# Performance work log

Measured on AMD Instinct MI355X. Metric: run time of the kernel, lower is better.

The kernel has to match this reference:

```python
import jax, jax.numpy as jnp
import numpy as np

B, T = 8, 8192
D_X, D_H, D_K, D_V = 256, 512, 128, 128
RES_DIMS = [128, 128, 128, 128]
R = sum(RES_DIMS)
MEM_SLOTS, EP_TOPK = 256, 8
LN_EPS = 1e-5


def _ln(x, g, b):
    m = x.mean(-1, keepdims=True)
    v = ((x - m) ** 2).mean(-1, keepdims=True)
    return (x - m) * jax.lax.rsqrt(v + LN_EPS) * g + b


def _l2norm(x, eps=1e-8):
    return x / jnp.maximum(jnp.linalg.norm(x, axis=-1, keepdims=True), eps)


def setup_inputs() -> dict:
    key = jax.random.key(0)
    ks = jax.random.split(key, 12)
    def w(k, shape):  # xavier-ish scaling
        return jax.random.normal(k, shape, jnp.float32) * (shape[-1] ** -0.5)
    return dict(
        x_seq=jax.random.normal(ks[0], (B, T, D_X), jnp.float32),
        Wx_w=w(ks[1], (R, D_X)), Wx_b=jnp.zeros((R,), jnp.float32),
        Wh_w=w(ks[2], (R, D_H)),
        res_alpha=jnp.full((len(RES_DIMS),), -1.0, jnp.float32),
        A_scale=jnp.ones((D_H,), jnp.float32),
        B_w=w(ks[3], (D_H, R)),
        U_w=w(ks[4], (D_H, D_X)), U_b=jnp.zeros((D_H,), jnp.float32),
        fftn_g=jnp.ones((D_H,), jnp.float32), fftn_b=jnp.zeros((D_H,), jnp.float32),
        fftp_w=w(ks[5], (D_H, D_H)), fftp_b=jnp.zeros((D_H,), jnp.float32),
        fft_mix=jnp.asarray(0.5, jnp.float32),
        mix_logit=jnp.asarray(0.0, jnp.float32),
        key_w=w(ks[6], (D_K, R + D_X)), key_b=jnp.zeros((D_K,), jnp.float32),
        val_w=w(ks[7], (D_V, D_H)), val_b=jnp.zeros((D_V,), jnp.float32),
        rm_w=w(ks[8], (D_H, D_V)), rm_b=jnp.zeros((D_H,), jnp.float32),
        rn_g=jnp.ones((R,), jnp.float32), rn_b=jnp.zeros((R,), jnp.float32),
        mem_keys=jax.random.normal(ks[9], (B, MEM_SLOTS, D_K), jnp.float32),
        mem_vals=jax.random.normal(ks[10], (B, MEM_SLOTS, D_K), jnp.float32),
        heb_H=jax.random.normal(ks[11], (B, D_K, D_V), jnp.float32) * 0.1,
    )


def reference(x_seq, Wx_w, Wx_b, Wh_w, res_alpha, A_scale, B_w, U_w, U_b,
              fftn_g, fftn_b, fftp_w, fftp_b, fft_mix, mix_logit,
              key_w, key_b, val_w, val_b, rm_w, rm_b, rn_g, rn_b,
              mem_keys, mem_vals, heb_H):
    b = x_seq.shape[0]
    seg_index = np.repeat(np.arange(len(RES_DIMS)), RES_DIMS)  # static (R,)
    h_prev = jnp.zeros((b, D_H), x_seq.dtype)  # h0 = None
    r_prev = jnp.zeros((b, R), x_seq.dtype)    # r0 = None

    # reservoir update (fully parallel over T since h_prev/r_prev are broadcast)
    Wx = jnp.einsum('btx,rx->btr', x_seq, Wx_w) + Wx_b
    Wh = (h_prev @ Wh_w.T)[:, None, :]                    # (B,1,R), no bias in fwd
    alpha = jax.nn.sigmoid(res_alpha)[seg_index]          # (R,)
    r_seq = alpha * r_prev[:, None, :] + (1.0 - alpha) * jnp.tanh(Wx + Wh)
    r_seq = _ln(r_seq, rn_g, rn_b)

    # core state
    Ah = A_scale * h_prev[:, None, :]
    Bh = jnp.einsum('btr,hr->bth', r_seq, B_w)
    Uh = jnp.einsum('btx,hx->bth', x_seq, U_w) + U_b
    h_tilde = jax.nn.gelu(Ah + Bh + Uh, approximate=False)

    # FFT feature mixing
    h_norm = _ln(h_tilde, fftn_g, fftn_b)
    s = jax.nn.sigmoid(fft_mix)
    h_freq = jnp.fft.rfft(h_norm, n=D_H, axis=-1, norm='ortho')
    h_ifft = jnp.fft.irfft(h_freq * s, n=D_H, axis=-1, norm='ortho')
    h_fft_out = jnp.einsum('bth,oh->bto', h_ifft, fftp_w) + fftp_b
    hs = (1.0 - s) * h_tilde + s * h_fft_out

    # memory recall (once per sequence, batched)
    k = jnp.einsum('btf,kf->btk', jnp.concatenate([r_seq, x_seq], axis=-1), key_w) + key_b
    v = jnp.einsum('bth,vh->btv', hs, val_w) + val_b  # as in original (used for auto_write)
    c = _l2norm(k)
    q = c.mean(axis=1)                                # (B,d_k)

    # episodic: cosine top-k over slots, softmax-weighted value read
    kn = _l2norm(mem_keys)
    sim = jnp.einsum('bk,bmk->bm', _l2norm(q), kn)
    top_sim, top_idx = jax.lax.top_k(sim, EP_TOPK)
    w_att = jax.nn.softmax(top_sim, axis=-1)
    vals = jnp.take_along_axis(mem_vals, top_idx[..., None], axis=1)  # (B,topk,d_v)
    v_hat = jnp.einsum('bk,bkv->bv', w_att, vals)

    # hebbian: linear associative read from per-batch outer-product memory
    v_hebb = jnp.einsum('bk,bkv->bv', q, heb_H)

    mix = jax.nn.sigmoid(mix_logit)
    v_comb = mix * v_hat + (1.0 - mix) * v_hebb
    h_mem = v_comb @ rm_w.T + rm_b                    # (B,d_h)
    hs = hs + 0.5 * h_mem[:, None, :]
    return hs, r_seq
```

## Files before the change

### kernel.cpp

```cpp
#include <hip/hip_runtime.h>
#include <cmath>


typedef __attribute__((ext_vector_type(8)))  short short8;
typedef __attribute__((ext_vector_type(16))) float f32x16;

__device__ __forceinline__ unsigned short f2bf(float f) {
  union { float f; unsigned u; } v; v.f = f;
  unsigned r = v.u + 0x7FFF + ((v.u >> 16) & 1);
  return (unsigned short)(r >> 16);
}
__device__ __forceinline__ float bf2f(unsigned short h) {
  union { unsigned u; float f; } v; v.u = ((unsigned)h) << 16; return v.f;
}
__device__ __forceinline__ f32x16 mfma16(short8 a, short8 b, f32x16 c) {
  return __builtin_amdgcn_mfma_f32_32x32x16_bf16(a, b, c, 0, 0, 0);
}
__device__ __forceinline__ void barrier_lgkm() {
  asm volatile("s_waitcnt lgkmcnt(0)" ::: "memory");
  __builtin_amdgcn_s_barrier();
  __builtin_amdgcn_sched_barrier(0);
}

__global__ __launch_bounds__(256) void k_wconv(
    const float* __restrict__ wx, const float* __restrict__ key,
    const float* __restrict__ bw, const float* __restrict__ uw,
    const float* __restrict__ fftpw, const float* __restrict__ fg,
    unsigned short* __restrict__ wxp, unsigned short* __restrict__ keyp,
    unsigned short* __restrict__ bwp, unsigned short* __restrict__ uwp,
    unsigned short* __restrict__ fftps) {
  int i = blockIdx.x * 256 + threadIdx.x;
  if (i >= 884736) return;
  float v; int n, k, N; unsigned short* dst;
  if (i < 131072)      { int j = i;          N = 512; k = j & 255; n = j >> 8; v = wx[j];  dst = wxp; }
  else if (i < 229376) { int j = i - 131072; N = 128; k = j % 768; n = j / 768; v = key[j]; dst = keyp; }
  else if (i < 491520) { int j = i - 229376; N = 512; k = j & 511; n = j >> 9; v = bw[j];  dst = bwp; }
  else if (i < 622592) { int j = i - 491520; N = 512; k = j & 255; n = j >> 8; v = uw[j];  dst = uwp; }
  else                 { int j = i - 622592; N = 512; k = j & 511; n = j >> 9; v = fftpw[j] * fg[k]; dst = fftps; }
  dst[(k >> 5) * (N * 32) + ((k >> 3) & 3) * (N * 8) + n * 8 + (k & 7)] = f2bf(v);
}

__global__ __launch_bounds__(512, 4) void k_rk(
    const float* __restrict__ x, const unsigned short* __restrict__ wxp,
    const unsigned short* __restrict__ keyp,
    const float* __restrict__ wxb, const float* __restrict__ resa,
    const float* __restrict__ rng, const float* __restrict__ rnb,
    const float* __restrict__ keyb,
    float* __restrict__ rout, float* __restrict__ partial) {
  __shared__ short sX[8192];
  __shared__ short sR[16384];
  __shared__ float red[640];
  const int t = threadIdx.x, w = t >> 6, lane = t & 63, lr = lane & 31, lh = lane >> 5;
  const int m0 = blockIdx.x * 32;

#pragma unroll
  for (int i = 0; i < 4; ++i) {
    int c = t + i * 512;
    int row = c >> 6, k0 = (c & 63) * 4;
    float4 v = *reinterpret_cast<const float4*>(x + (size_t)(m0 + row) * 256 + k0);
    uint2 p;
    p.x = (unsigned)f2bf(v.x) | ((unsigned)f2bf(v.y) << 16);
    p.y = (unsigned)f2bf(v.z) | ((unsigned)f2bf(v.w) << 16);
    *reinterpret_cast<uint2*>(&sX[(k0 >> 3) * 256 + row * 8 + (k0 & 7)]) = p;
  }
  barrier_lgkm();

  f32x16 acc[2];
#pragma unroll
  for (int ni = 0; ni < 2; ++ni)
#pragma unroll
    for (int e = 0; e < 16; ++e) acc[ni][e] = 0.f;
  short8 b0[4], b1[4];
  auto loadB0 = [&](int s, short8 (&bd)[4]) {
#pragma unroll
    for (int kh = 0; kh < 2; ++kh)
#pragma unroll
      for (int ni = 0; ni < 2; ++ni)
        bd[kh * 2 + ni] = *reinterpret_cast<const short8*>(
            wxp + (size_t)s * 16384 + (kh * 2 + lh) * 4096 + (64 * w + 32 * ni + lr) * 8);
  };
  auto mf0 = [&](int s, short8 (&bc)[4]) {
    short8 af[2];
#pragma unroll
    for (int kh = 0; kh < 2; ++kh)
      af[kh] = *reinterpret_cast<const short8*>(&sX[(s * 4 + kh * 2 + lh) * 256 + lr * 8]);
    __builtin_amdgcn_s_setprio(1);
#pragma unroll
    for (int kh = 0; kh < 2; ++kh)
#pragma unroll
      for (int ni = 0; ni < 2; ++ni)
        acc[ni] = mfma16(af[kh], bc[kh * 2 + ni], acc[ni]);
    __builtin_amdgcn_s_setprio(0);
  };
  loadB0(0, b0);
  for (int s = 0; s < 8; s += 2) {
    loadB0(s + 1, b1);
    mf0(s, b0);
    if (s + 2 < 8) loadB0(s + 2, b0);
    mf0(s + 1, b1);
  }

#pragma unroll
  for (int ni = 0; ni < 2; ++ni) {
    int col = 64 * w + 32 * ni + lr;
    float al = 1.f / (1.f + expf(-resa[col >> 7]));
    float oma = 1.f - al, bbv = wxb[col];
#pragma unroll
    for (int r = 0; r < 16; ++r)
      acc[ni][r] = oma * tanhf(acc[ni][r] + bbv);
  }
#pragma unroll
  for (int r = 0; r < 16; ++r) {
    float s1 = acc[0][r] + acc[1][r];
    float s2 = acc[0][r] * acc[0][r] + acc[1][r] * acc[1][r];
#pragma unroll
    for (int m = 1; m <= 16; m <<= 1) { s1 += __shfl_xor(s1, m); s2 += __shfl_xor(s2, m); }
    int rl = (r & 3) + 8 * (r >> 2) + 4 * lh;
    if (lr == r) { red[w * 32 + rl] = s1; red[256 + w * 32 + rl] = s2; }
  }
  __syncthreads();
  if (t < 32) {
    float s1 = 0.f, s2 = 0.f;
#pragma unroll
    for (int n = 0; n < 8; ++n) { s1 += red[n * 32 + t]; s2 += red[256 + n * 32 + t]; }
    float mean = s1 * (1.f / 512.f);
    float var = s2 * (1.f / 512.f) - mean * mean;
    float rstd = rsqrtf(var + 1e-5f);
    red[512 + t * 2] = mean;
    red[512 + t * 2 + 1] = rstd;
  }
  __syncthreads();
#pragma unroll
  for (int q = 0; q < 4; ++q) {
    float4 stA = *reinterpret_cast<float4*>(&red[512 + (8 * q + 4 * lh) * 2]);
    float4 stB = *reinterpret_cast<float4*>(&red[512 + (8 * q + 4 * lh) * 2 + 4]);
    float mean[4] = {stA.x, stA.z, stB.x, stB.z};
    float rstd[4] = {stA.y, stA.w, stB.y, stB.w};
#pragma unroll
    for (int ni = 0; ni < 2; ++ni) {
      int col = 64 * w + 32 * ni + lr;
      float g = rng[col], bbv = rnb[col];
#pragma unroll
      for (int e = 0; e < 4; ++e) {
        int r = 4 * q + e;
        int rloc = 8 * q + 4 * lh + e;
        float val = (acc[ni][r] - mean[e]) * rstd[e] * g + bbv;
        rout[(size_t)(m0 + rloc) * 512 + col] = val;
        sR[(col >> 3) * 256 + rloc * 8 + (col & 7)] = (short)f2bf(val);
      }
    }
  }
  barrier_lgkm();

  const int g = w >> 2, nw2 = w & 3;
  f32x16 ak;
#pragma unroll
  for (int e = 0; e < 16; ++e) ak[e] = 0.f;
  short8 kb0[2], kb1[2];
  auto loadBk = [&](int gc, short8 (&bd)[2]) {
#pragma unroll
    for (int kh = 0; kh < 2; ++kh)
      bd[kh] = *reinterpret_cast<const short8*>(
          keyp + (size_t)gc * 4096 + (kh * 2 + lh) * 1024 + (32 * nw2 + lr) * 8);
  };
  auto mfk = [&](int gc, short8 (&bc)[2]) {
    const short* P = (gc < 16) ? sR : sX;
    int sb = (gc < 16) ? gc * 4 : (gc - 16) * 4;
    short8 af[2];
#pragma unroll
    for (int kh = 0; kh < 2; ++kh)
      af[kh] = *reinterpret_cast<const short8*>(&P[(sb + kh * 2 + lh) * 256 + lr * 8]);
    __builtin_amdgcn_s_setprio(1);
#pragma unroll
    for (int kh = 0; kh < 2; ++kh)
      ak = mfma16(af[kh], bc[kh], ak);
    __builtin_amdgcn_s_setprio(0);
  };
  const int gbase = g * 12;
  loadBk(gbase, kb0);
  for (int s = 0; s < 12; s += 2) {
    loadBk(gbase + s + 1, kb1);
    mfk(gbase + s, kb0);
    if (s + 2 < 12) loadBk(gbase + s + 2, kb0);
    mfk(gbase + s + 1, kb1);
  }
  __syncthreads();
  float* kp = reinterpret_cast<float*>(sR);
#pragma unroll
  for (int r = 0; r < 16; ++r) {
    int rr = (r & 3) + 8 * (r >> 2) + 4 * lh;
    kp[g * 4096 + rr * 128 + nw2 * 32 + lr] = ak[r];
  }
  __syncthreads();
  {
    int rr = t >> 4, cg = t & 15;
    float s1 = 0.f;
#pragma unroll
    for (int j = 0; j < 8; ++j) {
      int c = cg * 8 + j;
      float v = kp[rr * 128 + c] + kp[4096 + rr * 128 + c] + keyb[c];
      s1 += v * v;
    }
#pragma unroll
    for (int m = 1; m <= 8; m <<= 1) s1 += __shfl_xor(s1, m);
    if (cg == 0) red[rr] = 1.f / fmaxf(sqrtf(s1), 1e-8f);
  }
  __syncthreads();
  if (t < 128) {
    float p = 0.f;
    float bb = keyb[t];
#pragma unroll 4
    for (int rr = 0; rr < 32; ++rr)
      p += (kp[rr * 128 + t] + kp[4096 + rr * 128 + t] + bb) * red[rr];
    partial[(size_t)blockIdx.x * 128 + t] = p;
  }
}

__global__ __launch_bounds__(256) void k_qred(const float* __restrict__ partial,
                                              float* __restrict__ q_ws) {
  int gid = blockIdx.x * 256 + threadIdx.x;
  int b = gid >> 7, c = gid & 127;
  float s = 0.f;
  for (int i = 0; i < 256; ++i) s += partial[(size_t)(b * 256 + i) * 128 + c];
  q_ws[gid] = s * (1.f / 8192.f);
}

__global__ __launch_bounds__(256) void k_cvec(const float* __restrict__ fb,
                                              const float* __restrict__ fftpw,
                                              float* __restrict__ cvec) {
  int o = blockIdx.x * 256 + threadIdx.x;
  const float* w = fftpw + (size_t)o * 512;
  float s = 0.f;
  for (int k = 0; k < 512; ++k) s += fb[k] * w[k];
  cvec[o] = s;
}

__global__ __launch_bounds__(256) void k_mem(
    const float* __restrict__ q_ws, const float* __restrict__ mkeys,
    const float* __restrict__ mvals, const float* __restrict__ hebH,
    const float* __restrict__ rmw, const float* __restrict__ rmb,
    const float* __restrict__ mixl, float* __restrict__ hm) {
  const int b = blockIdx.x, t = threadIdx.x;
  __shared__ float qv[128];
  __shared__ float ssim[256];
  __shared__ float red[256];
  __shared__ float tval[8];
  __shared__ int tidx[8];
  __shared__ float wsm[8];
  __shared__ float vcs[128];

  if (t < 128) qv[t] = q_ws[b * 128 + t];
  __syncthreads();
  red[t] = (t < 128) ? qv[t] * qv[t] : 0.f;
  __syncthreads();
  for (int s = 128; s > 0; s >>= 1) {
    if (t < s) red[t] += red[t + s];
    __syncthreads();
  }
  float qsc = 1.f / fmaxf(sqrtf(red[0]), 1e-8f);
  {
    const float* mk = mkeys + ((size_t)b * 256 + t) * 128;
    float dot = 0.f, ms = 0.f;
    for (int k = 0; k < 128; ++k) { float mv = mk[k]; dot += qv[k] * mv; ms += mv * mv; }
    ssim[t] = dot * qsc / fmaxf(sqrtf(ms), 1e-8f);
  }
  __syncthreads();
  for (int it = 0; it < 8; ++it) {
    if (t < 64) {
      float bv = -1e30f; int bi = 0;
#pragma unroll
      for (int u = 0; u < 4; ++u) {
        int m = t * 4 + u;
        float v = ssim[m];
        if (v > bv) { bv = v; bi = m; }
      }
      for (int off = 32; off; off >>= 1) {
        float ov = __shfl_xor(bv, off, 64);
        int oi = __shfl_xor(bi, off, 64);
        if (ov > bv || (ov == bv && oi < bi)) { bv = ov; bi = oi; }
      }
      if (t == 0) { tval[it] = bv; tidx[it] = bi; ssim[bi] = -1e30f; }
    }
    __syncthreads();
  }
  if (t == 0) {
    float m0 = tval[0], sum = 0.f, e[8];
#pragma unroll
    for (int i = 0; i < 8; ++i) { e[i] = expf(tval[i] - m0); sum += e[i]; }
#pragma unroll
    for (int i = 0; i < 8; ++i) wsm[i] = e[i] / sum;
  }
  __syncthreads();
  float mix = 1.f / (1.f + expf(-mixl[0]));
  if (t < 128) {
    float vh = 0.f;
#pragma unroll
    for (int i = 0; i < 8; ++i) vh += wsm[i] * mvals[((size_t)b * 256 + tidx[i]) * 128 + t];
    float vhb = 0.f;
    const float* H = hebH + (size_t)b * 128 * 128;
    for (int k = 0; k < 128; ++k) vhb += qv[k] * H[k * 128 + t];
    vcs[t] = mix * vh + (1.f - mix) * vhb;
  }
  __syncthreads();
  for (int h = t; h < 512; h += 256) {
    float sum = rmb[h];
    const float* wr = rmw + (size_t)h * 128;
    for (int v = 0; v < 128; ++v) sum += vcs[v] * wr[v];
    hm[b * 512 + h] = sum;
  }
}

__global__ __launch_bounds__(512, 4) void k_fused(
    const float* __restrict__ rseq, const float* __restrict__ x,
    const unsigned short* __restrict__ bwp, const unsigned short* __restrict__ uwp,
    const float* __restrict__ ub, const unsigned short* __restrict__ fftps,
    const float* __restrict__ fftpb, const float* __restrict__ fmix,
    const float* __restrict__ cvec, const float* __restrict__ hm,
    float* __restrict__ hs) {
  __shared__ short sX[8192];
  __shared__ short sR[16384];
  __shared__ float red[640];
  const int t = threadIdx.x, w = t >> 6, lane = t & 63, lr = lane & 31, lh = lane >> 5;
  const int m0 = blockIdx.x * 32;
  const int bidx = m0 >> 13;

#pragma unroll
  for (int i = 0; i < 8; ++i) {
    int c = t + i * 512;
    int row = c >> 7, k0 = (c & 127) * 4;
    float4 v = *reinterpret_cast<const float4*>(rseq + (size_t)(m0 + row) * 512 + k0);
    uint2 p;
    p.x = (unsigned)f2bf(v.x) | ((unsigned)f2bf(v.y) << 16);
    p.y = (unsigned)f2bf(v.z) | ((unsigned)f2bf(v.w) << 16);
    *reinterpret_cast<uint2*>(&sR[(k0 >> 3) * 256 + row * 8 + (k0 & 7)]) = p;
  }
#pragma unroll
  for (int i = 0; i < 4; ++i) {
    int c = t + i * 512;
    int row = c >> 6, k0 = (c & 63) * 4;
    float4 v = *reinterpret_cast<const float4*>(x + (size_t)(m0 + row) * 256 + k0);
    uint2 p;
    p.x = (unsigned)f2bf(v.x) | ((unsigned)f2bf(v.y) << 16);
    p.y = (unsigned)f2bf(v.z) | ((unsigned)f2bf(v.w) << 16);
    *reinterpret_cast<uint2*>(&sX[(k0 >> 3) * 256 + row * 8 + (k0 & 7)]) = p;
  }
  barrier_lgkm();

  f32x16 acc[2];
#pragma unroll
  for (int ni = 0; ni < 2; ++ni)
#pragma unroll
    for (int e = 0; e < 16; ++e) acc[ni][e] = 0.f;
  short8 b0[4], b1[4];
  auto loadB1 = [&](int s, short8 (&bd)[4]) {
    const unsigned short* wp = (s < 16) ? (bwp + (size_t)s * 16384)
                                        : (uwp + (size_t)(s - 16) * 16384);
#pragma unroll
    for (int kh = 0; kh < 2; ++kh)
#pragma unroll
      for (int ni = 0; ni < 2; ++ni)
        bd[kh * 2 + ni] = *reinterpret_cast<const short8*>(
            wp + (kh * 2 + lh) * 4096 + (64 * w + 32 * ni + lr) * 8);
  };
  auto mf1 = [&](int s, short8 (&bc)[4]) {
    const short* P = (s < 16) ? sR : sX;
    int sb = (s < 16) ? s * 4 : (s - 16) * 4;
    short8 af[2];
#pragma unroll
    for (int kh = 0; kh < 2; ++kh)
      af[kh] = *reinterpret_cast<const short8*>(&P[(sb + kh * 2 + lh) * 256 + lr * 8]);
    __builtin_amdgcn_s_setprio(1);
#pragma unroll
    for (int kh = 0; kh < 2; ++kh)
#pragma unroll
      for (int ni = 0; ni < 2; ++ni)
        acc[ni] = mfma16(af[kh], bc[kh * 2 + ni], acc[ni]);
    __builtin_amdgcn_s_setprio(0);
  };
  loadB1(0, b0);
  for (int s = 0; s < 24; s += 2) {
    loadB1(s + 1, b1);
    mf1(s, b0);
    if (s + 2 < 24) loadB1(s + 2, b0);
    mf1(s + 1, b1);
  }

#pragma unroll
  for (int ni = 0; ni < 2; ++ni) {
    int col = 64 * w + 32 * ni + lr;
    float ubc = ub[col];
#pragma unroll
    for (int r = 0; r < 16; ++r) {
      float pre = acc[ni][r] + ubc;
      acc[ni][r] = 0.5f * pre * (1.f + erff(pre * 0.70710678118654752f));
    }
  }
#pragma unroll
  for (int r = 0; r < 16; ++r) {
    float s1 = acc[0][r] + acc[1][r];
    float s2 = acc[0][r] * acc[0][r] + acc[1][r] * acc[1][r];
#pragma unroll
    for (int m = 1; m <= 16; m <<= 1) { s1 += __shfl_xor(s1, m); s2 += __shfl_xor(s2, m); }
    int rl = (r & 3) + 8 * (r >> 2) + 4 * lh;
    if (lr == r) { red[w * 32 + rl] = s1; red[256 + w * 32 + rl] = s2; }
  }
  __syncthreads();
  if (t < 32) {
    float s1 = 0.f, s2 = 0.f;
#pragma unroll
    for (int n = 0; n < 8; ++n) { s1 += red[n * 32 + t]; s2 += red[256 + n * 32 + t]; }
    float mean = s1 * (1.f / 512.f);
    float var = s2 * (1.f / 512.f) - mean * mean;
    float rstd = rsqrtf(var + 1e-5f);
    red[512 + t * 2] = mean;
    red[512 + t * 2 + 1] = rstd;
  }
  __syncthreads();
  unsigned htp[2][8];
#pragma unroll
  for (int ni = 0; ni < 2; ++ni)
#pragma unroll
    for (int p = 0; p < 8; ++p)
      htp[ni][p] = (unsigned)f2bf(acc[ni][2 * p]) |
                   ((unsigned)f2bf(acc[ni][2 * p + 1]) << 16);
  auto loadB2 = [&](int s, short8 (&bd)[4]) {
#pragma unroll
    for (int kh = 0; kh < 2; ++kh)
#pragma unroll
      for (int ni = 0; ni < 2; ++ni)
        bd[kh * 2 + ni] = *reinterpret_cast<const short8*>(
            fftps + (size_t)s * 16384 + (kh * 2 + lh) * 4096 + (64 * w + 32 * ni + lr) * 8);
  };
  loadB2(0, b0);
#pragma unroll
  for (int q = 0; q < 4; ++q) {
    float4 stA = *reinterpret_cast<float4*>(&red[512 + (8 * q + 4 * lh) * 2]);
    float4 stB = *reinterpret_cast<float4*>(&red[512 + (8 * q + 4 * lh) * 2 + 4]);
    float mean[4] = {stA.x, stA.z, stB.x, stB.z};
    float rstd[4] = {stA.y, stA.w, stB.y, stB.w};
#pragma unroll
    for (int ni = 0; ni < 2; ++ni) {
      int col = 64 * w + 32 * ni + lr;
#pragma unroll
      for (int e = 0; e < 4; ++e) {
        int r = 4 * q + e;
        float z = (acc[ni][r] - mean[e]) * rstd[e];
        int rloc = 8 * q + 4 * lh + e;
        sR[(col >> 3) * 256 + rloc * 8 + (col & 7)] = (short)f2bf(z);
      }
    }
  }
#pragma unroll
  for (int ni = 0; ni < 2; ++ni)
#pragma unroll
    for (int e = 0; e < 16; ++e) acc[ni][e] = 0.f;
  barrier_lgkm();

  auto mf2 = [&](int s, short8 (&bc)[4]) {
    short8 af[2];
#pragma unroll
    for (int kh = 0; kh < 2; ++kh)
      af[kh] = *reinterpret_cast<const short8*>(&sR[(s * 4 + kh * 2 + lh) * 256 + lr * 8]);
    __builtin_amdgcn_s_setprio(1);
#pragma unroll
    for (int kh = 0; kh < 2; ++kh)
#pragma unroll
      for (int ni = 0; ni < 2; ++ni)
        acc[ni] = mfma16(af[kh], bc[kh * 2 + ni], acc[ni]);
    __builtin_amdgcn_s_setprio(0);
  };
  for (int s = 0; s < 16; s += 2) {
    loadB2(s + 1, b1);
    mf2(s, b0);
    if (s + 2 < 16) loadB2(s + 2, b0);
    mf2(s + 1, b1);
  }

  const float sg = 1.f / (1.f + expf(-fmix[0]));
  const float s2f = sg * sg, oms = 1.f - sg;
#pragma unroll
  for (int ni = 0; ni < 2; ++ni) {
    int col = 64 * w + 32 * ni + lr;
    float base = s2f * cvec[col] + sg * fftpb[col] + 0.5f * hm[bidx * 512 + col];
#pragma unroll
    for (int p = 0; p < 8; ++p) {
      unsigned pk = htp[ni][p];
      int r0 = 2 * p;
      int rloc = (r0 & 3) + 8 * (r0 >> 2) + 4 * lh;
      float o0 = oms * bf2f((unsigned short)(pk & 0xFFFF)) + s2f * acc[ni][r0] + base;
      float o1 = oms * bf2f((unsigned short)(pk >> 16)) + s2f * acc[ni][r0 + 1] + base;
      hs[(size_t)(m0 + rloc) * 512 + col] = o0;
      hs[(size_t)(m0 + rloc + 1) * 512 + col] = o1;
    }
  }
}

extern "C" void kernel_launch(void* const* d_in, const int* in_sizes, int n_in,
                              void* d_out, int out_size, void* d_ws, size_t ws_size,
                              hipStream_t stream) {
  (void)in_sizes; (void)n_in; (void)out_size; (void)ws_size;
  const float* x     = (const float*)d_in[0];
  const float* Wxw   = (const float*)d_in[1];
  const float* Wxb   = (const float*)d_in[2];
  const float* resa  = (const float*)d_in[4];
  const float* Bw    = (const float*)d_in[6];
  const float* Uw    = (const float*)d_in[7];
  const float* Ub    = (const float*)d_in[8];
  const float* fg    = (const float*)d_in[9];
  const float* fb    = (const float*)d_in[10];
  const float* fftpw = (const float*)d_in[11];
  const float* fftpb = (const float*)d_in[12];
  const float* fmix  = (const float*)d_in[13];
  const float* mixl  = (const float*)d_in[14];
  const float* keyw  = (const float*)d_in[15];
  const float* keyb  = (const float*)d_in[16];
  const float* rmw   = (const float*)d_in[19];
  const float* rmb   = (const float*)d_in[20];
  const float* rng   = (const float*)d_in[21];
  const float* rnb   = (const float*)d_in[22];
  const float* mkeys = (const float*)d_in[23];
  const float* mvals = (const float*)d_in[24];
  const float* hebH  = (const float*)d_in[25];

  float* outp = (float*)d_out;
  float* hs   = outp;
  float* rout = outp + (size_t)65536 * 512;

  unsigned short* wsu = (unsigned short*)d_ws;
  unsigned short* wxp    = wsu;
  unsigned short* keyp   = wsu + 131072;
  unsigned short* bwp    = wsu + 229376;
  unsigned short* uwp    = wsu + 491520;
  unsigned short* fftps  = wsu + 622592;
  float* wsf     = (float*)d_ws;
  float* partial = wsf + 524288;
  float* q_ws    = wsf + 786432;
  float* hm      = wsf + 787456;
  float* cvec    = wsf + 791552;

  k_wconv<<<3456, 256, 0, stream>>>(Wxw, keyw, Bw, Uw, fftpw, fg,
                                    wxp, keyp, bwp, uwp, fftps);
  k_cvec <<<2,    256, 0, stream>>>(fb, fftpw, cvec);
  k_rk   <<<2048, 512, 0, stream>>>(x, wxp, keyp, Wxb, resa, rng, rnb, keyb,
                                    rout, partial);
  k_qred <<<4,    256, 0, stream>>>(partial, q_ws);
  k_mem  <<<8,    256, 0, stream>>>(q_ws, mkeys, mvals, hebH, rmw, rmb, mixl, hm);
  k_fused<<<2048, 512, 0, stream>>>(rout, x, bwp, uwp, Ub, fftps, fftpb,
                                    fmix, cvec, hm, hs);
}
```

Before: 309.0 us.

## Double k_fused row tile to 64 rows so each weight fragment feeds two MFMAs

Raises the fused kernel's M tile from 32 to 64 rows per block. Each wave now holds a 2x2 grid of accumulators and reuses every loaded B-weight fragment across two row sub-tiles, which halves the weight traffic from global/L2 per output row. In exchange the block needs twice the LDS and registers, so launch bounds drop to 2 blocks per CU and the grid halves to 1024 blocks. That lowers occupancy and latency hiding.

```diff
diff --git a/kernel.cpp b/kernel.cpp
--- a/kernel.cpp
+++ b/kernel.cpp
@@ -310,47 +310,49 @@
   }
 }
 
-__global__ __launch_bounds__(512, 4) void k_fused(
+__global__ __launch_bounds__(512, 2) void k_fused(
     const float* __restrict__ rseq, const float* __restrict__ x,
     const unsigned short* __restrict__ bwp, const unsigned short* __restrict__ uwp,
     const float* __restrict__ ub, const unsigned short* __restrict__ fftps,
     const float* __restrict__ fftpb, const float* __restrict__ fmix,
     const float* __restrict__ cvec, const float* __restrict__ hm,
     float* __restrict__ hs) {
-  __shared__ short sX[8192];
-  __shared__ short sR[16384];
-  __shared__ float red[640];
+  __shared__ short sR[32768];
+  __shared__ short sX[16384];
+  __shared__ float red[1152];
   const int t = threadIdx.x, w = t >> 6, lane = t & 63, lr = lane & 31, lh = lane >> 5;
-  const int m0 = blockIdx.x * 32;
+  const int m0 = blockIdx.x * 64;
   const int bidx = m0 >> 13;
 
 #pragma unroll
-  for (int i = 0; i < 8; ++i) {
+  for (int i = 0; i < 16; ++i) {
     int c = t + i * 512;
     int row = c >> 7, k0 = (c & 127) * 4;
     float4 v = *reinterpret_cast<const float4*>(rseq + (size_t)(m0 + row) * 512 + k0);
     uint2 p;
     p.x = (unsigned)f2bf(v.x) | ((unsigned)f2bf(v.y) << 16);
     p.y = (unsigned)f2bf(v.z) | ((unsigned)f2bf(v.w) << 16);
-    *reinterpret_cast<uint2*>(&sR[(k0 >> 3) * 256 + row * 8 + (k0 & 7)]) = p;
-  }
-#pragma unroll
-  for (int i = 0; i < 4; ++i) {
+    *reinterpret_cast<uint2*>(&sR[(k0 >> 3) * 512 + row * 8 + (k0 & 7)]) = p;
+  }
+#pragma unroll
+  for (int i = 0; i < 8; ++i) {
     int c = t + i * 512;
     int row = c >> 6, k0 = (c & 63) * 4;
     float4 v = *reinterpret_cast<const float4*>(x + (size_t)(m0 + row) * 256 + k0);
     uint2 p;
     p.x = (unsigned)f2bf(v.x) | ((unsigned)f2bf(v.y) << 16);
     p.y = (unsigned)f2bf(v.z) | ((unsigned)f2bf(v.w) << 16);
-    *reinterpret_cast<uint2*>(&sX[(k0 >> 3) * 256 + row * 8 + (k0 & 7)]) = p;
+    *reinterpret_cast<uint2*>(&sX[(k0 >> 3) * 512 + row * 8 + (k0 & 7)]) = p;
   }
   barrier_lgkm();
 
-  f32x16 acc[2];
-#pragma unroll
-  for (int ni = 0; ni < 2; ++ni)
-#pragma unroll
-    for (int e = 0; e < 16; ++e) acc[ni][e] = 0.f;
+  f32x16 acc[2][2];
+#pragma unroll
+  for (int mi = 0; mi < 2; ++mi)
+#pragma unroll
+    for (int ni = 0; ni < 2; ++ni)
+#pragma unroll
+      for (int e = 0; e < 16; ++e) acc[mi][ni][e] = 0.f;
   short8 b0[4], b1[4];
   auto loadB1 = [&](int s, short8 (&bd)[4]) {
     const unsigned short* wp = (s < 16) ? (bwp + (size_t)s * 16384)
@@ -365,16 +367,21 @@
   auto mf1 = [&](int s, short8 (&bc)[4]) {
     const short* P = (s < 16) ? sR : sX;
     int sb = (s < 16) ? s * 4 : (s - 16) * 4;
-    short8 af[2];
-#pragma unroll
-    for (int kh = 0; kh < 2; ++kh)
-      af[kh] = *reinterpret_cast<const short8*>(&P[(sb + kh * 2 + lh) * 256 + lr * 8]);
+    short8 af[2][2];
+#pragma unroll
+    for (int kh = 0; kh < 2; ++kh)
+#pragma unroll
+      for (int mi = 0; mi < 2; ++mi)
+        af[kh][mi] = *reinterpret_cast<const short8*>(
+            &P[(sb + kh * 2 + lh) * 512 + (32 * mi + lr) * 8]);
     __builtin_amdgcn_s_setprio(1);
 #pragma unroll
     for (int kh = 0; kh < 2; ++kh)
 #pragma unroll
-      for (int ni = 0; ni < 2; ++ni)
-        acc[ni] = mfma16(af[kh], bc[kh * 2 + ni], acc[ni]);
+      for (int mi = 0; mi < 2; ++mi)
+#pragma unroll
+        for (int ni = 0; ni < 2; ++ni)
+          acc[mi][ni] = mfma16(af[kh][mi], bc[kh * 2 + ni], acc[mi][ni]);
     __builtin_amdgcn_s_setprio(0);
   };
   loadB1(0, b0);
@@ -386,43 +393,50 @@
   }
 
 #pragma unroll
-  for (int ni = 0; ni < 2; ++ni) {
-    int col = 64 * w + 32 * ni + lr;
-    float ubc = ub[col];
+  for (int mi = 0; mi < 2; ++mi)
+#pragma unroll
+    for (int ni = 0; ni < 2; ++ni) {
+      int col = 64 * w + 32 * ni + lr;
+      float ubc = ub[col];
+#pragma unroll
+      for (int r = 0; r < 16; ++r) {
+        float pre = acc[mi][ni][r] + ubc;
+        acc[mi][ni][r] = 0.5f * pre * (1.f + erff(pre * 0.70710678118654752f));
+      }
+    }
+#pragma unroll
+  for (int mi = 0; mi < 2; ++mi)
 #pragma unroll
     for (int r = 0; r < 16; ++r) {
-      float pre = acc[ni][r] + ubc;
-      acc[ni][r] = 0.5f * pre * (1.f + erff(pre * 0.70710678118654752f));
-    }
-  }
-#pragma unroll
-  for (int r = 0; r < 16; ++r) {
-    float s1 = acc[0][r] + acc[1][r];
-    float s2 = acc[0][r] * acc[0][r] + acc[1][r] * acc[1][r];
-#pragma unroll
-    for (int m = 1; m <= 16; m <<= 1) { s1 += __shfl_xor(s1, m); s2 += __shfl_xor(s2, m); }
-    int rl = (r & 3) + 8 * (r >> 2) + 4 * lh;
-    if (lr == r) { red[w * 32 + rl] = s1; red[256 + w * 32 + rl] = s2; }
-  }
-  __syncthreads();
-  if (t < 32) {
+      float s1 = acc[mi][0][r] + acc[mi][1][r];
+      float s2 = acc[mi][0][r] * acc[mi][0][r] + acc[mi][1][r] * acc[mi][1][r];
+#pragma unroll
+      for (int m = 1; m <= 16; m <<= 1) { s1 += __shfl_xor(s1, m); s2 += __shfl_xor(s2, m); }
+      int rl = (r & 3) + 8 * (r >> 2) + 4 * lh;
+      if (lr == r) { red[(w * 2 + mi) * 32 + rl] = s1; red[512 + (w * 2 + mi) * 32 + rl] = s2; }
+    }
+  __syncthreads();
+  if (t < 64) {
+    int mi = t >> 5, rl = t & 31;
     float s1 = 0.f, s2 = 0.f;
 #pragma unroll
-    for (int n = 0; n < 8; ++n) { s1 += red[n * 32 + t]; s2 += red[256 + n * 32 + t]; }
+    for (int n = 0; n < 8; ++n) { s1 += red[(n * 2 + mi) * 32 + rl]; s2 += red[512 + (n * 2 + mi) * 32 + rl]; }
     float mean = s1 * (1.f / 512.f);
     float var = s2 * (1.f / 512.f) - mean * mean;
     float rstd = rsqrtf(var + 1e-5f);
-    red[512 + t * 2] = mean;
-    red[512 + t * 2 + 1] = rstd;
-  }
-  __syncthreads();
-  unsigned htp[2][8];
-#pragma unroll
-  for (int ni = 0; ni < 2; ++ni)
-#pragma unroll
-    for (int p = 0; p < 8; ++p)
-      htp[ni][p] = (unsigned)f2bf(acc[ni][2 * p]) |
-                   ((unsigned)f2bf(acc[ni][2 * p + 1]) << 16);
+    red[1024 + t * 2] = mean;
+    red[1024 + t * 2 + 1] = rstd;
+  }
+  __syncthreads();
+  unsigned htp[2][2][8];
+#pragma unroll
+  for (int mi = 0; mi < 2; ++mi)
+#pragma unroll
+    for (int ni = 0; ni < 2; ++ni)
+#pragma unroll
+      for (int p = 0; p < 8; ++p)
+        htp[mi][ni][p] = (unsigned)f2bf(acc[mi][ni][2 * p]) |
+                         ((unsigned)f2bf(acc[mi][ni][2 * p + 1]) << 16);
   auto loadB2 = [&](int s, short8 (&bd)[4]) {
 #pragma unroll
     for (int kh = 0; kh < 2; ++kh)
@@ -433,40 +447,49 @@
   };
   loadB2(0, b0);
 #pragma unroll
-  for (int q = 0; q < 4; ++q) {
-    float4 stA = *reinterpret_cast<float4*>(&red[512 + (8 * q + 4 * lh) * 2]);
-    float4 stB = *reinterpret_cast<float4*>(&red[512 + (8 * q + 4 * lh) * 2 + 4]);
-    float mean[4] = {stA.x, stA.z, stB.x, stB.z};
-    float rstd[4] = {stA.y, stA.w, stB.y, stB.w};
-#pragma unroll
-    for (int ni = 0; ni < 2; ++ni) {
-      int col = 64 * w + 32 * ni + lr;
-#pragma unroll
-      for (int e = 0; e < 4; ++e) {
-        int r = 4 * q + e;
-        float z = (acc[ni][r] - mean[e]) * rstd[e];
-        int rloc = 8 * q + 4 * lh + e;
-        sR[(col >> 3) * 256 + rloc * 8 + (col & 7)] = (short)f2bf(z);
+  for (int q = 0; q < 4; ++q)
+#pragma unroll
+    for (int mi = 0; mi < 2; ++mi) {
+      float4 stA = *reinterpret_cast<float4*>(&red[1024 + (32 * mi + 8 * q + 4 * lh) * 2]);
+      float4 stB = *reinterpret_cast<float4*>(&red[1024 + (32 * mi + 8 * q + 4 * lh) * 2 + 4]);
+      float mean[4] = {stA.x, stA.z, stB.x, stB.z};
+      float rstd[4] = {stA.y, stA.w, stB.y, stB.w};
+#pragma unroll
+      for (int ni = 0; ni < 2; ++ni) {
+        int col = 64 * w + 32 * ni + lr;
+#pragma unroll
+        for (int e = 0; e < 4; ++e) {
+          int r = 4 * q + e;
+          float z = (acc[mi][ni][r] - mean[e]) * rstd[e];
+          int rloc = 32 * mi + 8 * q + 4 * lh + e;
+          sR[(col >> 3) * 512 + rloc * 8 + (col & 7)] = (short)f2bf(z);
+        }
       }
     }
-  }
-#pragma unroll
-  for (int ni = 0; ni < 2; ++ni)
-#pragma unroll
-    for (int e = 0; e < 16; ++e) acc[ni][e] = 0.f;
+#pragma unroll
+  for (int mi = 0; mi < 2; ++mi)
+#pragma unroll
+    for (int ni = 0; ni < 2; ++ni)
+#pragma unroll
+      for (int e = 0; e < 16; ++e) acc[mi][ni][e] = 0.f;
   barrier_lgkm();
 
   auto mf2 = [&](int s, short8 (&bc)[4]) {
-    short8 af[2];
-#pragma unroll
-    for (int kh = 0; kh < 2; ++kh)
-      af[kh] = *reinterpret_cast<const short8*>(&sR[(s * 4 + kh * 2 + lh) * 256 + lr * 8]);
+    short8 af[2][2];
+#pragma unroll
+    for (int kh = 0; kh < 2; ++kh)
+#pragma unroll
+      for (int mi = 0; mi < 2; ++mi)
+        af[kh][mi] = *reinterpret_cast<const short8*>(
+            &sR[(s * 4 + kh * 2 + lh) * 512 + (32 * mi + lr) * 8]);
     __builtin_amdgcn_s_setprio(1);
 #pragma unroll
     for (int kh = 0; kh < 2; ++kh)
 #pragma unroll
-      for (int ni = 0; ni < 2; ++ni)
-        acc[ni] = mfma16(af[kh], bc[kh * 2 + ni], acc[ni]);
+      for (int mi = 0; mi < 2; ++mi)
+#pragma unroll
+        for (int ni = 0; ni < 2; ++ni)
+          acc[mi][ni] = mfma16(af[kh][mi], bc[kh * 2 + ni], acc[mi][ni]);
     __builtin_amdgcn_s_setprio(0);
   };
   for (int s = 0; s < 16; s += 2) {
@@ -479,20 +502,22 @@
   const float sg = 1.f / (1.f + expf(-fmix[0]));
   const float s2f = sg * sg, oms = 1.f - sg;
 #pragma unroll
-  for (int ni = 0; ni < 2; ++ni) {
-    int col = 64 * w + 32 * ni + lr;
-    float base = s2f * cvec[col] + sg * fftpb[col] + 0.5f * hm[bidx * 512 + col];
-#pragma unroll
-    for (int p = 0; p < 8; ++p) {
-      unsigned pk = htp[ni][p];
-      int r0 = 2 * p;
-      int rloc = (r0 & 3) + 8 * (r0 >> 2) + 4 * lh;
-      float o0 = oms * bf2f((unsigned short)(pk & 0xFFFF)) + s2f * acc[ni][r0] + base;
-      float o1 = oms * bf2f((unsigned short)(pk >> 16)) + s2f * acc[ni][r0 + 1] + base;
-      hs[(size_t)(m0 + rloc) * 512 + col] = o0;
-      hs[(size_t)(m0 + rloc + 1) * 512 + col] = o1;
-    }
-  }
+  for (int mi = 0; mi < 2; ++mi)
+#pragma unroll
+    for (int ni = 0; ni < 2; ++ni) {
+      int col = 64 * w + 32 * ni + lr;
+      float base = s2f * cvec[col] + sg * fftpb[col] + 0.5f * hm[bidx * 512 + col];
+#pragma unroll
+      for (int p = 0; p < 8; ++p) {
+        unsigned pk = htp[mi][ni][p];
+        int r0 = 2 * p;
+        int rloc = 32 * mi + (r0 & 3) + 8 * (r0 >> 2) + 4 * lh;
+        float o0 = oms * bf2f((unsigned short)(pk & 0xFFFF)) + s2f * acc[mi][ni][r0] + base;
+        float o1 = oms * bf2f((unsigned short)(pk >> 16)) + s2f * acc[mi][ni][r0 + 1] + base;
+        hs[(size_t)(m0 + rloc) * 512 + col] = o0;
+        hs[(size_t)(m0 + rloc + 1) * 512 + col] = o1;
+      }
+    }
 }
 
 extern "C" void kernel_launch(void* const* d_in, const int* in_sizes, int n_in,
@@ -545,6 +570,6 @@
                                     rout, partial);
   k_qred <<<4,    256, 0, stream>>>(partial, q_ws);
   k_mem  <<<8,    256, 0, stream>>>(q_ws, mkeys, mvals, hebH, rmw, rmb, mixl, hm);
-  k_fused<<<2048, 512, 0, stream>>>(rout, x, bwp, uwp, Ub, fftps, fftpb,
+  k_fused<<<1024, 512, 0, stream>>>(rout, x, bwp, uwp, Ub, fftps, fftpb,
                                     fmix, cvec, hm, hs);
 }
```

Measured after the change: 341.5 us. 1.11x slower.
